# Optimization experiments

Hardware: AMD Instinct MI355X
Metric: run time of the kernel (lower is better)

The kernel has to match this reference:

```python
import jax, jax.numpy as jnp
import numpy as np

B, S, H, I, E = 4, 4096, 1024, 4096, 4
VOCAB = 32000


def setup_inputs() -> dict:
    key = jax.random.key(0)
    k1, k2, k3, k4, k5 = jax.random.split(key, 5)
    scale = 1.0 / np.sqrt(H)
    return {
        "hidden_states": jax.random.normal(k1, (B, S, H), dtype=jnp.float32),
        "gate_proj": jax.random.normal(k2, (E, H, I), dtype=jnp.float32) * scale,
        "up_proj": jax.random.normal(k3, (E, H, I), dtype=jnp.float32) * scale,
        "down_proj": jax.random.normal(k4, (E, I, H), dtype=jnp.float32) * (1.0 / np.sqrt(I)),
        "token_ids": jax.random.randint(k5, (B, S), 0, VOCAB, dtype=jnp.int64),
    }


def reference(hidden_states, gate_proj, up_proj, down_proj, token_ids):
    # hidden_states: [B, S, H]; token_ids: [B, S]
    num_experts = gate_proj.shape[0]
    expert_ids = token_ids % num_experts  # [B, S]
    out = jnp.zeros_like(hidden_states)
    for e in range(num_experts):  # small fixed expert loop
        gate = jax.nn.silu(jnp.einsum("bsh,hi->bsi", hidden_states, gate_proj[e]))
        up = jnp.einsum("bsh,hi->bsi", hidden_states, up_proj[e])
        y = jnp.einsum("bsi,ih->bsh", gate * up, down_proj[e])
        out = jnp.where((expert_ids == e)[..., None], y, out)
    return out
```

## Files before the change

### kernel.cpp

```cpp
#include <hip/hip_runtime.h>

#define TOK    16384
#define HD     1024
#define ID     4096
#define NE     4
#define MAXMT  131
#define MAXMT2 67

typedef __attribute__((ext_vector_type(4))) float f32x4;
typedef __attribute__((ext_vector_type(8))) short bf16x8;
typedef unsigned int u32;

static __device__ __forceinline__ unsigned short f2bf(float f) {
  unsigned u = __float_as_uint(f);
  u += 0x7FFFu + ((u >> 16) & 1u);
  return (unsigned short)(u >> 16);
}

static __device__ __forceinline__ void gl16(const void* g, void* l) {
  __builtin_amdgcn_global_load_lds((const __attribute__((address_space(1))) u32*)g,
                                   (__attribute__((address_space(3))) u32*)l, 16, 0, 0);
}

static __device__ __forceinline__ void barx() {
  asm volatile("" ::: "memory");
  __builtin_amdgcn_s_barrier();
  asm volatile("" ::: "memory");
}

__global__ void k_route0(const int* __restrict__ ids, int* __restrict__ meta) {
  __shared__ int cnt[4];
  int t = threadIdx.x;
  if (t < 4) cnt[t] = 0;
  __syncthreads();
  int l0 = 0, l1 = 0, l2 = 0, l3 = 0;
  for (int i = t; i < TOK; i += 256) {
    int e = ids[i] & 3;
    l0 += (e == 0); l1 += (e == 1); l2 += (e == 2); l3 += (e == 3);
  }
  atomicAdd(&cnt[0], l0); atomicAdd(&cnt[1], l1);
  atomicAdd(&cnt[2], l2); atomicAdd(&cnt[3], l3);
  __syncthreads();
  if (t == 0) {
    int o = 0;
    for (int e = 0; e < 4; ++e) { meta[e] = o; meta[8 + e] = o; o += cnt[e]; }
    meta[4] = o;
  }
}

__global__ void k_route1(const int* __restrict__ ids, int* __restrict__ meta,
                         int* __restrict__ perm) {
  int i = blockIdx.x * 256 + threadIdx.x;
  if (i < TOK) {
    int e = ids[i] & 3;
    int s = atomicAdd(&meta[8 + e], 1);
    perm[s] = i;
  }
}

__global__ void k_conv(const float* __restrict__ s, unsigned short* __restrict__ d, int n8) {
  int i = blockIdx.x * blockDim.x + threadIdx.x;
  int st = gridDim.x * blockDim.x;
  for (; i < n8; i += st) {
    const f32x4* p = (const f32x4*)(s + ((size_t)i << 3));
    f32x4 a = p[0], b = p[1];
    union { unsigned short u[8]; uint4 q; } o;
    o.u[0] = f2bf(a.x); o.u[1] = f2bf(a.y); o.u[2] = f2bf(a.z); o.u[3] = f2bf(a.w);
    o.u[4] = f2bf(b.x); o.u[5] = f2bf(b.y); o.u[6] = f2bf(b.z); o.u[7] = f2bf(b.w);
    *(uint4*)(d + ((size_t)i << 3)) = o.q;
  }
}

__global__ void k_tr(const float* __restrict__ src, unsigned short* __restrict__ dst,
                     int R, int C) {
  __shared__ float tile[64][65];
  size_t mo = (size_t)blockIdx.z * R * C;
  const float* s = src + mo;
  unsigned short* d = dst + mo;
  int r0 = blockIdx.y << 6, c0 = blockIdx.x << 6;
  int t = threadIdx.x;
  int lr = t >> 4, lc = (t & 15) << 2;
  #pragma unroll
  for (int it = 0; it < 4; ++it) {
    int r = lr + (it << 4);
    f32x4 v = *(const f32x4*)(s + (size_t)(r0 + r) * C + c0 + lc);
    tile[r][lc] = v.x; tile[r][lc + 1] = v.y; tile[r][lc + 2] = v.z; tile[r][lc + 3] = v.w;
  }
  __syncthreads();
  int c = t >> 2, rb = (t & 3) << 4;
  union { unsigned short u[16]; uint4 q[2]; } o;
  #pragma unroll
  for (int j = 0; j < 16; ++j) o.u[j] = f2bf(tile[rb + j][c]);
  uint4* dp = (uint4*)(d + (size_t)(c0 + c) * R + r0 + rb);
  dp[0] = o.q[0]; dp[1] = o.q[1];
}

#define MFMA16 __builtin_amdgcn_mfma_f32_16x16x32_bf16

__global__ __launch_bounds__(512, 2) void k_gemm1(
    const unsigned short* __restrict__ hid,
    const unsigned short* __restrict__ gT,
    const unsigned short* __restrict__ uT,
    const int* __restrict__ meta,
    const int* __restrict__ perm,
    unsigned short* __restrict__ act) {
  extern __shared__ __align__(16) char smem[];
  int offs[5];
  #pragma unroll
  for (int i = 0; i < 5; ++i) offs[i] = meta[i];
  int mt = blockIdx.x;
  int e = -1, mloc = 0, base = 0;
  #pragma unroll
  for (int ee = 0; ee < 4; ++ee) {
    int tiles = (offs[ee + 1] - offs[ee] + 255) >> 8;
    if (e < 0 && mt < base + tiles) { e = ee; mloc = mt - base; }
    base += tiles;
  }
  if (e < 0) return;
  int slot0 = offs[e] + (mloc << 8);
  int send = offs[e + 1];
  int tid = threadIdx.x, lane = tid & 63, wid = tid >> 6;
  int n0 = blockIdx.y << 7;

  int ke = (((tid & 7) ^ ((tid >> 3) & 7)) << 3);
  int rloc = tid >> 3;
  const unsigned short* srcA[4];
  #pragma unroll
  for (int i = 0; i < 4; ++i) {
    int slot = slot0 + i * 64 + rloc;
    int pr = perm[slot < send ? slot : slot0];
    srcA[i] = hid + (size_t)pr * HD + ke;
  }
  const unsigned short* gb = gT + (size_t)e * ID * HD;
  const unsigned short* ub = uT + (size_t)e * ID * HD;
  const unsigned short* srcG[2];
  const unsigned short* srcU[2];
  #pragma unroll
  for (int i = 0; i < 2; ++i) {
    int row = n0 + i * 64 + rloc;
    srcG[i] = gb + (size_t)row * HD + ke;
    srcU[i] = ub + (size_t)row * HD + ke;
  }
  int dstA[4], dstG[2], dstU[2];
  #pragma unroll
  for (int i = 0; i < 4; ++i) dstA[i] = i * 8192 + wid * 1024;
  #pragma unroll
  for (int i = 0; i < 2; ++i) { dstG[i] = 32768 + i * 8192 + wid * 1024;
                                dstU[i] = 49152 + i * 8192 + wid * 1024; }

  int wm = wid >> 1, wn = wid & 1;
  int r16 = lane & 15, kg = lane >> 4;
  int offA[4], offG[4], offU[4];
  #pragma unroll
  for (int m = 0; m < 4; ++m) {
    int row = wm * 64 + m * 16 + r16;
    offA[m] = row * 128 + ((kg << 4) ^ ((row & 7) << 4));
  }
  #pragma unroll
  for (int n = 0; n < 4; ++n) {
    int row = wn * 64 + n * 16 + r16;
    int o = row * 128 + ((kg << 4) ^ ((row & 7) << 4));
    offG[n] = 32768 + o;
    offU[n] = 49152 + o;
  }

  f32x4 zero = {0.f, 0.f, 0.f, 0.f};
  f32x4 ag[4][4], au[4][4];
  #pragma unroll
  for (int m = 0; m < 4; ++m)
    #pragma unroll
    for (int n = 0; n < 4; ++n) { ag[m][n] = zero; au[m][n] = zero; }

  {
    char* b = smem;
    #pragma unroll
    for (int i = 0; i < 4; ++i) gl16(srcA[i], b + dstA[i]);
    #pragma unroll
    for (int i = 0; i < 2; ++i) gl16(srcG[i], b + dstG[i]);
    #pragma unroll
    for (int i = 0; i < 2; ++i) gl16(srcU[i], b + dstU[i]);
  }

  #pragma unroll 2
  for (int t = 0; t < HD / 64; ++t) {
    const char* bc = smem + (t & 1) * 65536;
    if (t < HD / 64 - 1) {
      char* bn = smem + ((t + 1) & 1) * 65536;
      int ko = (t + 1) * 64;
      #pragma unroll
      for (int i = 0; i < 4; ++i) gl16(srcA[i] + ko, bn + dstA[i]);
      #pragma unroll
      for (int i = 0; i < 2; ++i) gl16(srcG[i] + ko, bn + dstG[i]);
      #pragma unroll
      for (int i = 0; i < 2; ++i) gl16(srcU[i] + ko, bn + dstU[i]);
      asm volatile("s_waitcnt vmcnt(8)" ::: "memory");
    } else {
      asm volatile("s_waitcnt vmcnt(0)" ::: "memory");
    }
    barx();

    bf16x8 fa[4], fg[4], fu[4];
    #pragma unroll
    for (int m = 0; m < 4; ++m) fa[m] = *(const bf16x8*)(bc + offA[m]);
    #pragma unroll
    for (int n = 0; n < 4; ++n) fg[n] = *(const bf16x8*)(bc + offG[n]);
    barx();
    asm volatile("s_waitcnt lgkmcnt(0)" ::: "memory");
    __builtin_amdgcn_sched_barrier(0);
    __builtin_amdgcn_s_setprio(1);
    #pragma unroll
    for (int m = 0; m < 4; ++m)
      #pragma unroll
      for (int n = 0; n < 4; ++n)
        ag[m][n] = MFMA16(fa[m], fg[n], ag[m][n], 0, 0, 0);
    __builtin_amdgcn_s_setprio(0);
    barx();
    #pragma unroll
    for (int n = 0; n < 4; ++n) fu[n] = *(const bf16x8*)(bc + offU[n]);
    barx();
    asm volatile("s_waitcnt lgkmcnt(0)" ::: "memory");
    __builtin_amdgcn_sched_barrier(0);
    __builtin_amdgcn_s_setprio(1);
    #pragma unroll
    for (int m = 0; m < 4; ++m)
      #pragma unroll
      for (int n = 0; n < 4; ++n)
        au[m][n] = MFMA16(fa[m], fu[n], au[m][n], 0, 0, 0);
    __builtin_amdgcn_s_setprio(0);
    barx();
    #pragma unroll
    for (int m = 0; m < 4; ++m) fa[m] = *(const bf16x8*)(bc + (offA[m] ^ 64));
    #pragma unroll
    for (int n = 0; n < 4; ++n) fg[n] = *(const bf16x8*)(bc + (offG[n] ^ 64));
    barx();
    asm volatile("s_waitcnt lgkmcnt(0)" ::: "memory");
    __builtin_amdgcn_sched_barrier(0);
    __builtin_amdgcn_s_setprio(1);
    #pragma unroll
    for (int m = 0; m < 4; ++m)
      #pragma unroll
      for (int n = 0; n < 4; ++n)
        ag[m][n] = MFMA16(fa[m], fg[n], ag[m][n], 0, 0, 0);
    __builtin_amdgcn_s_setprio(0);
    barx();
    #pragma unroll
    for (int n = 0; n < 4; ++n) fu[n] = *(const bf16x8*)(bc + (offU[n] ^ 64));
    barx();
    asm volatile("s_waitcnt lgkmcnt(0)" ::: "memory");
    __builtin_amdgcn_sched_barrier(0);
    __builtin_amdgcn_s_setprio(1);
    #pragma unroll
    for (int m = 0; m < 4; ++m)
      #pragma unroll
      for (int n = 0; n < 4; ++n)
        au[m][n] = MFMA16(fa[m], fu[n], au[m][n], 0, 0, 0);
    __builtin_amdgcn_s_setprio(0);
    barx();
  }

  #pragma unroll
  for (int m = 0; m < 4; ++m) {
    int lr = wm * 64 + m * 16 + kg * 4;
    #pragma unroll
    for (int n = 0; n < 4; ++n) {
      int col = n0 + wn * 64 + n * 16 + r16;
      #pragma unroll
      for (int r = 0; r < 4; ++r) {
        int slot = slot0 + lr + r;
        if (slot < send) {
          float g = ag[m][n][r];
          float u = au[m][n][r];
          float y = (g / (1.f + __expf(-g))) * u;
          act[(size_t)slot * ID + col] = f2bf(y);
        }
      }
    }
  }
}

__global__ __launch_bounds__(256, 2) void k_gemm2(
    const unsigned short* __restrict__ act,
    const unsigned short* __restrict__ dT,
    const int* __restrict__ meta,
    const int* __restrict__ perm,
    float* __restrict__ out) {
  __shared__ unsigned short As[128 * 64];
  __shared__ unsigned short Bs[128 * 64];
  int offs[5];
  #pragma unroll
  for (int i = 0; i < 5; ++i) offs[i] = meta[i];
  int mt = blockIdx.x;
  int e = -1, mloc = 0, base = 0;
  #pragma unroll
  for (int ee = 0; ee < 4; ++ee) {
    int tiles = (offs[ee + 1] - offs[ee] + 127) >> 7;
    if (e < 0 && mt < base + tiles) { e = ee; mloc = mt - base; }
    base += tiles;
  }
  if (e < 0) return;
  int slot0 = offs[e] + (mloc << 7);
  int send = offs[e + 1];
  int tid = threadIdx.x;
  int n0 = blockIdx.y << 7;
  const unsigned short* dbase = dT + (size_t)e * HD * ID;
  const unsigned short* ap[4];
  const unsigned short* bp[4];
  int wofs[4];
  #pragma unroll
  for (int it = 0; it < 4; ++it) {
    int b = (tid << 4) + (it << 12);
    int row = b >> 7;
    int kob = b & 127;
    int slot = slot0 + row;
    int s2 = slot < send ? slot : slot0;
    ap[it] = act + (size_t)s2 * ID + (kob >> 1);
    bp[it] = dbase + (size_t)(n0 + row) * ID + (kob >> 1);
    wofs[it] = row * 64 + ((kob ^ ((row & 7) << 4)) >> 1);
  }
  int lane = tid & 63, wid = tid >> 6;
  int wm = wid >> 1, wn = wid & 1;
  int r16 = lane & 15, kg = lane >> 4;
  f32x4 zero = {0.f, 0.f, 0.f, 0.f};
  f32x4 acc[4][4];
  #pragma unroll
  for (int m = 0; m < 4; ++m)
    #pragma unroll
    for (int n = 0; n < 4; ++n) acc[m][n] = zero;

  bf16x8 sa[4], sb[4];
  #pragma unroll
  for (int it = 0; it < 4; ++it) {
    sa[it] = *(const bf16x8*)(ap[it]);
    sb[it] = *(const bf16x8*)(bp[it]);
  }
  for (int kt = 0; kt < ID / 64; ++kt) {
    __syncthreads();
    #pragma unroll
    for (int it = 0; it < 4; ++it) {
      *(bf16x8*)(As + wofs[it]) = sa[it];
      *(bf16x8*)(Bs + wofs[it]) = sb[it];
    }
    __syncthreads();
    if (kt < ID / 64 - 1) {
      int ko = (kt + 1) << 6;
      #pragma unroll
      for (int it = 0; it < 4; ++it) {
        sa[it] = *(const bf16x8*)(ap[it] + ko);
        sb[it] = *(const bf16x8*)(bp[it] + ko);
      }
    }
    #pragma unroll
    for (int kk = 0; kk < 2; ++kk) {
      bf16x8 fa[4], fb[4];
      #pragma unroll
      for (int m = 0; m < 4; ++m) {
        int row = (wm << 6) + (m << 4) + r16;
        int kob = (kk << 6) + (kg << 4);
        fa[m] = *(const bf16x8*)(As + row * 64 + ((kob ^ ((row & 7) << 4)) >> 1));
      }
      #pragma unroll
      for (int n = 0; n < 4; ++n) {
        int row = (wn << 6) + (n << 4) + r16;
        int kob = (kk << 6) + (kg << 4);
        fb[n] = *(const bf16x8*)(Bs + row * 64 + ((kob ^ ((row & 7) << 4)) >> 1));
      }
      #pragma unroll
      for (int m = 0; m < 4; ++m)
        #pragma unroll
        for (int n = 0; n < 4; ++n)
          acc[m][n] = __builtin_amdgcn_mfma_f32_16x16x32_bf16(fa[m], fb[n], acc[m][n], 0, 0, 0);
    }
  }
  #pragma unroll
  for (int m = 0; m < 4; ++m) {
    int lr = (wm << 6) + (m << 4) + (kg << 2);
    int pr4[4];
    #pragma unroll
    for (int r = 0; r < 4; ++r) {
      int slot = slot0 + lr + r;
      pr4[r] = slot < send ? perm[slot] : -1;
    }
    #pragma unroll
    for (int n = 0; n < 4; ++n) {
      int col = n0 + (wn << 6) + (n << 4) + r16;
      #pragma unroll
      for (int r = 0; r < 4; ++r) {
        if (pr4[r] >= 0) out[(size_t)pr4[r] * HD + col] = acc[m][n][r];
      }
    }
  }
}

extern "C" void kernel_launch(void* const* d_in, const int* in_sizes, int n_in,
                              void* d_out, int out_size, void* d_ws, size_t ws_size,
                              hipStream_t stream) {
  const float* hs = (const float*)d_in[0];
  const float* gw = (const float*)d_in[1];
  const float* uw = (const float*)d_in[2];
  const float* dw = (const float*)d_in[3];
  const int* ids = (const int*)d_in[4];
  float* out = (float*)d_out;

  char* w = (char*)d_ws;
  size_t o = 0;
  int* meta = (int*)(w + o); o += 64;
  int* perm = (int*)(w + o); o += (size_t)TOK * 4;
  o = (o + 255) & ~(size_t)255;
  unsigned short* hid = (unsigned short*)(w + o); o += (size_t)TOK * HD * 2;
  unsigned short* gT  = (unsigned short*)(w + o); o += (size_t)NE * ID * HD * 2;
  unsigned short* uT  = (unsigned short*)(w + o); o += (size_t)NE * ID * HD * 2;
  unsigned short* dT  = (unsigned short*)(w + o); o += (size_t)NE * ID * HD * 2;
  unsigned short* actb = (unsigned short*)(w + o); o += (size_t)TOK * ID * 2;

  hipFuncSetAttribute((const void*)k_gemm1,
                      hipFuncAttributeMaxDynamicSharedMemorySize, 131072);

  hipLaunchKernelGGL(k_route0, dim3(1), dim3(256), 0, stream, ids, meta);
  hipLaunchKernelGGL(k_route1, dim3(TOK / 256), dim3(256), 0, stream, ids, meta, perm);
  hipLaunchKernelGGL(k_conv, dim3(2048), dim3(256), 0, stream, hs, hid, TOK * HD / 8);
  hipLaunchKernelGGL(k_tr, dim3(ID / 64, HD / 64, NE), dim3(256), 0, stream, gw, gT, HD, ID);
  hipLaunchKernelGGL(k_tr, dim3(ID / 64, HD / 64, NE), dim3(256), 0, stream, uw, uT, HD, ID);
  hipLaunchKernelGGL(k_tr, dim3(HD / 64, ID / 64, NE), dim3(256), 0, stream, dw, dT, ID, HD);
  hipLaunchKernelGGL(k_gemm1, dim3(MAXMT2, ID / 128), dim3(512), 131072, stream,
                     hid, gT, uT, meta, perm, actb);
  hipLaunchKernelGGL(k_gemm2, dim3(MAXMT, HD / 128), dim3(256), 0, stream,
                     actb, dT, meta, perm, out);
}
```

Before: 767.7 us.

## Restructure gate/up GEMM into unified 256x256 tile with interleaved staging

The gate and up weight tiles are interleaved into one B operand, so each wave computes a 128x64 output block with 8x4 accumulators. Global-to-LDS staging is split into half-tile pieces and interleaved between MFMA phases within a manually unrolled double-buffered loop. Both GEMMs now use a 1-D grid remapped so that consecutive blocks are spread across 8 groups (XCD-aware swizzle) for better L2 reuse. The three transpose launches are merged into a single kernel. Register pressure and tricky waitcnt accounting are the main risks.

```diff
diff --git a/kernel.cpp b/kernel.cpp
--- a/kernel.cpp
+++ b/kernel.cpp
@@ -6,6 +6,7 @@
 #define NE     4
 #define MAXMT  131
 #define MAXMT2 67
+#define NKT    (HD / 64)
 
 typedef __attribute__((ext_vector_type(4))) float f32x4;
 typedef __attribute__((ext_vector_type(8))) short bf16x8;
@@ -71,13 +72,25 @@
   }
 }
 
-__global__ void k_tr(const float* __restrict__ src, unsigned short* __restrict__ dst,
-                     int R, int C) {
+__global__ void k_tr12(const float* __restrict__ gw, const float* __restrict__ uw,
+                       const float* __restrict__ dw, unsigned short* __restrict__ gT,
+                       unsigned short* __restrict__ uT, unsigned short* __restrict__ dT) {
   __shared__ float tile[64][65];
-  size_t mo = (size_t)blockIdx.z * R * C;
-  const float* s = src + mo;
-  unsigned short* d = dst + mo;
-  int r0 = blockIdx.y << 6, c0 = blockIdx.x << 6;
+  int z = blockIdx.y;
+  const float* s; unsigned short* d; int R, C, lg;
+  if (z < 8) {
+    R = HD; C = ID; lg = 6;
+    int m = z & 3;
+    if (z < 4) { s = gw + (size_t)m * R * C; d = gT + (size_t)m * R * C; }
+    else       { s = uw + (size_t)m * R * C; d = uT + (size_t)m * R * C; }
+  } else {
+    R = ID; C = HD; lg = 4;
+    int m = z - 8;
+    s = dw + (size_t)m * R * C; d = dT + (size_t)m * R * C;
+  }
+  int bx = blockIdx.x;
+  int tx = bx & ((1 << lg) - 1), ty = bx >> lg;
+  int r0 = ty << 6, c0 = tx << 6;
   int t = threadIdx.x;
   int lr = t >> 4, lc = (t & 15) << 2;
   #pragma unroll
@@ -96,6 +109,23 @@
 }
 
 #define MFMA16 __builtin_amdgcn_mfma_f32_16x16x32_bf16
+
+#define RD_A(MH, KX, D) { _Pragma("unroll") for (int m = 0; m < 4; ++m) \
+  fa[m] = *(const bf16x8*)(smem + (D) + ((offA[m] + (MH) * 8192) ^ ((KX) << 6))); }
+#define RD_B(KX, D) { _Pragma("unroll") for (int n = 0; n < 4; ++n) \
+  fb[n] = *(const bf16x8*)(smem + (D) + (offB[n] ^ ((KX) << 6))); }
+#define STG_A(HH, TILE, D) { _Pragma("unroll") for (int j = (HH) * 2; j < (HH) * 2 + 2; ++j) \
+  gl16(srcA[j] + (TILE) * 64, smem + (D) + dstA[j]); }
+#define STG_B(HH, TILE, D) { _Pragma("unroll") for (int j = (HH) * 2; j < (HH) * 2 + 2; ++j) \
+  gl16(srcB[j] + (TILE) * 64, smem + (D) + dstB[j]); }
+#define PH_TAIL(MH) barx(); \
+  asm volatile("s_waitcnt lgkmcnt(0)" ::: "memory"); \
+  __builtin_amdgcn_sched_barrier(0); \
+  __builtin_amdgcn_s_setprio(1); \
+  { _Pragma("unroll") for (int m = 0; m < 4; ++m) \
+    _Pragma("unroll") for (int n = 0; n < 4; ++n) \
+      acc[(MH) * 4 + m][n] = MFMA16(fa[m], fb[n], acc[(MH) * 4 + m][n], 0, 0, 0); } \
+  __builtin_amdgcn_s_setprio(0)
 
 __global__ __launch_bounds__(512, 2) void k_gemm1(
     const unsigned short* __restrict__ hid,
@@ -108,7 +138,10 @@
   int offs[5];
   #pragma unroll
   for (int i = 0; i < 5; ++i) offs[i] = meta[i];
-  int mt = blockIdx.x;
+  int bid = blockIdx.x;
+  int logical = (bid & 7) * (MAXMT2 * 32 / 8) + (bid >> 3);
+  int mt = logical >> 5;
+  int ny = logical & 31;
   int e = -1, mloc = 0, base = 0;
   #pragma unroll
   for (int ee = 0; ee < 4; ++ee) {
@@ -120,156 +153,122 @@
   int slot0 = offs[e] + (mloc << 8);
   int send = offs[e + 1];
   int tid = threadIdx.x, lane = tid & 63, wid = tid >> 6;
-  int n0 = blockIdx.y << 7;
-
-  int ke = (((tid & 7) ^ ((tid >> 3) & 7)) << 3);
-  int rloc = tid >> 3;
+  int n0 = ny << 7;
+
+  int rsub = lane >> 3;
+  int ke = ((lane & 7) ^ rsub) << 3;
   const unsigned short* srcA[4];
-  #pragma unroll
-  for (int i = 0; i < 4; ++i) {
-    int slot = slot0 + i * 64 + rloc;
-    int pr = perm[slot < send ? slot : slot0];
-    srcA[i] = hid + (size_t)pr * HD + ke;
-  }
+  const unsigned short* srcB[4];
+  int dstA[4], dstB[4];
   const unsigned short* gb = gT + (size_t)e * ID * HD;
   const unsigned short* ub = uT + (size_t)e * ID * HD;
-  const unsigned short* srcG[2];
-  const unsigned short* srcU[2];
-  #pragma unroll
-  for (int i = 0; i < 2; ++i) {
-    int row = n0 + i * 64 + rloc;
-    srcG[i] = gb + (size_t)row * HD + ke;
-    srcU[i] = ub + (size_t)row * HD + ke;
-  }
-  int dstA[4], dstG[2], dstU[2];
-  #pragma unroll
-  for (int i = 0; i < 4; ++i) dstA[i] = i * 8192 + wid * 1024;
-  #pragma unroll
-  for (int i = 0; i < 2; ++i) { dstG[i] = 32768 + i * 8192 + wid * 1024;
-                                dstU[i] = 49152 + i * 8192 + wid * 1024; }
-
-  int wm = wid >> 1, wn = wid & 1;
+  #pragma unroll
+  for (int j = 0; j < 4; ++j) {
+    int r = j * 64 + wid * 8 + rsub;
+    int slot = slot0 + r;
+    int pr = perm[slot < send ? slot : slot0];
+    srcA[j] = hid + (size_t)pr * HD + ke;
+    dstA[j] = j * 8192 + wid * 1024;
+    int rb = r;
+    int s = rb >> 4;
+    int grow = n0 + ((s >> 1) << 4) + (rb & 15);
+    srcB[j] = ((s & 1) ? ub : gb) + (size_t)grow * HD + ke;
+    dstB[j] = 32768 + j * 8192 + wid * 1024;
+  }
+
+  int wm = wid >> 2, wn = wid & 3;
   int r16 = lane & 15, kg = lane >> 4;
-  int offA[4], offG[4], offU[4];
+  int offA[4], offB[4];
   #pragma unroll
   for (int m = 0; m < 4; ++m) {
-    int row = wm * 64 + m * 16 + r16;
+    int row = wm * 128 + m * 16 + r16;
     offA[m] = row * 128 + ((kg << 4) ^ ((row & 7) << 4));
   }
   #pragma unroll
   for (int n = 0; n < 4; ++n) {
     int row = wn * 64 + n * 16 + r16;
-    int o = row * 128 + ((kg << 4) ^ ((row & 7) << 4));
-    offG[n] = 32768 + o;
-    offU[n] = 49152 + o;
-  }
-
-  f32x4 zero = {0.f, 0.f, 0.f, 0.f};
-  f32x4 ag[4][4], au[4][4];
-  #pragma unroll
-  for (int m = 0; m < 4; ++m)
-    #pragma unroll
-    for (int n = 0; n < 4; ++n) { ag[m][n] = zero; au[m][n] = zero; }
-
+    offB[n] = 32768 + row * 128 + ((kg << 4) ^ ((row & 7) << 4));
+  }
+
+  f32x4 acc[8][4];
+  #pragma unroll
+  for (int m = 0; m < 8; ++m)
+    #pragma unroll
+    for (int n = 0; n < 4; ++n) acc[m][n] = (f32x4){0.f, 0.f, 0.f, 0.f};
+  bf16x8 fa[4], fb[4];
+
+  STG_B(0, 0, 0);
+  STG_A(0, 0, 0); STG_A(1, 0, 0);
+  STG_B(1, 0, 0);
+  STG_B(0, 1, 65536);
+  asm volatile("s_waitcnt vmcnt(2)" ::: "memory");
+  barx();
+
+  #pragma unroll 1
+  for (int i = 0; i < NKT / 2 - 1; ++i) {
+    int t1 = 2 * i + 1, t2 = 2 * i + 2, t3 = 2 * i + 3;
+    RD_A(0, 0, 0); RD_B(0, 0);
+    STG_B(1, t1, 65536);
+    PH_TAIL(0); barx();
+    RD_A(1, 0, 0);
+    STG_A(0, t1, 65536); STG_A(1, t1, 65536);
+    PH_TAIL(1); barx();
+    RD_A(0, 1, 0); RD_B(1, 0);
+    PH_TAIL(0); barx();
+    RD_A(1, 1, 0);
+    STG_B(0, t2, 0);
+    PH_TAIL(1);
+    asm volatile("s_waitcnt vmcnt(2)" ::: "memory");
+    barx();
+    RD_A(0, 0, 65536); RD_B(0, 65536);
+    STG_A(0, t2, 0); STG_A(1, t2, 0);
+    PH_TAIL(0); barx();
+    RD_A(1, 0, 65536);
+    STG_B(1, t2, 0);
+    PH_TAIL(1); barx();
+    RD_A(0, 1, 65536); RD_B(1, 65536);
+    PH_TAIL(0); barx();
+    RD_A(1, 1, 65536);
+    STG_B(0, t3, 65536);
+    PH_TAIL(1);
+    asm volatile("s_waitcnt vmcnt(2)" ::: "memory");
+    barx();
+  }
   {
-    char* b = smem;
-    #pragma unroll
-    for (int i = 0; i < 4; ++i) gl16(srcA[i], b + dstA[i]);
-    #pragma unroll
-    for (int i = 0; i < 2; ++i) gl16(srcG[i], b + dstG[i]);
-    #pragma unroll
-    for (int i = 0; i < 2; ++i) gl16(srcU[i], b + dstU[i]);
-  }
-
-  #pragma unroll 2
-  for (int t = 0; t < HD / 64; ++t) {
-    const char* bc = smem + (t & 1) * 65536;
-    if (t < HD / 64 - 1) {
-      char* bn = smem + ((t + 1) & 1) * 65536;
-      int ko = (t + 1) * 64;
-      #pragma unroll
-      for (int i = 0; i < 4; ++i) gl16(srcA[i] + ko, bn + dstA[i]);
-      #pragma unroll
-      for (int i = 0; i < 2; ++i) gl16(srcG[i] + ko, bn + dstG[i]);
-      #pragma unroll
-      for (int i = 0; i < 2; ++i) gl16(srcU[i] + ko, bn + dstU[i]);
-      asm volatile("s_waitcnt vmcnt(8)" ::: "memory");
-    } else {
-      asm volatile("s_waitcnt vmcnt(0)" ::: "memory");
-    }
+    RD_A(0, 0, 0); RD_B(0, 0);
+    STG_B(1, 15, 65536);
+    PH_TAIL(0); barx();
+    RD_A(1, 0, 0);
+    STG_A(0, 15, 65536); STG_A(1, 15, 65536);
+    PH_TAIL(1); barx();
+    RD_A(0, 1, 0); RD_B(1, 0);
+    PH_TAIL(0); barx();
+    RD_A(1, 1, 0);
+    PH_TAIL(1);
+    asm volatile("s_waitcnt vmcnt(0)" ::: "memory");
     barx();
-
-    bf16x8 fa[4], fg[4], fu[4];
-    #pragma unroll
-    for (int m = 0; m < 4; ++m) fa[m] = *(const bf16x8*)(bc + offA[m]);
-    #pragma unroll
-    for (int n = 0; n < 4; ++n) fg[n] = *(const bf16x8*)(bc + offG[n]);
-    barx();
-    asm volatile("s_waitcnt lgkmcnt(0)" ::: "memory");
-    __builtin_amdgcn_sched_barrier(0);
-    __builtin_amdgcn_s_setprio(1);
-    #pragma unroll
-    for (int m = 0; m < 4; ++m)
-      #pragma unroll
-      for (int n = 0; n < 4; ++n)
-        ag[m][n] = MFMA16(fa[m], fg[n], ag[m][n], 0, 0, 0);
-    __builtin_amdgcn_s_setprio(0);
-    barx();
-    #pragma unroll
-    for (int n = 0; n < 4; ++n) fu[n] = *(const bf16x8*)(bc + offU[n]);
-    barx();
-    asm volatile("s_waitcnt lgkmcnt(0)" ::: "memory");
-    __builtin_amdgcn_sched_barrier(0);
-    __builtin_amdgcn_s_setprio(1);
-    #pragma unroll
-    for (int m = 0; m < 4; ++m)
-      #pragma unroll
-      for (int n = 0; n < 4; ++n)
-        au[m][n] = MFMA16(fa[m], fu[n], au[m][n], 0, 0, 0);
-    __builtin_amdgcn_s_setprio(0);
-    barx();
-    #pragma unroll
-    for (int m = 0; m < 4; ++m) fa[m] = *(const bf16x8*)(bc + (offA[m] ^ 64));
-    #pragma unroll
-    for (int n = 0; n < 4; ++n) fg[n] = *(const bf16x8*)(bc + (offG[n] ^ 64));
-    barx();
-    asm volatile("s_waitcnt lgkmcnt(0)" ::: "memory");
-    __builtin_amdgcn_sched_barrier(0);
-    __builtin_amdgcn_s_setprio(1);
-    #pragma unroll
-    for (int m = 0; m < 4; ++m)
-      #pragma unroll
-      for (int n = 0; n < 4; ++n)
-        ag[m][n] = MFMA16(fa[m], fg[n], ag[m][n], 0, 0, 0);
-    __builtin_amdgcn_s_setprio(0);
-    barx();
-    #pragma unroll
-    for (int n = 0; n < 4; ++n) fu[n] = *(const bf16x8*)(bc + (offU[n] ^ 64));
-    barx();
-    asm volatile("s_waitcnt lgkmcnt(0)" ::: "memory");
-    __builtin_amdgcn_sched_barrier(0);
-    __builtin_amdgcn_s_setprio(1);
-    #pragma unroll
-    for (int m = 0; m < 4; ++m)
-      #pragma unroll
-      for (int n = 0; n < 4; ++n)
-        au[m][n] = MFMA16(fa[m], fu[n], au[m][n], 0, 0, 0);
-    __builtin_amdgcn_s_setprio(0);
-    barx();
-  }
-
-  #pragma unroll
-  for (int m = 0; m < 4; ++m) {
-    int lr = wm * 64 + m * 16 + kg * 4;
-    #pragma unroll
-    for (int n = 0; n < 4; ++n) {
-      int col = n0 + wn * 64 + n * 16 + r16;
+    RD_A(0, 0, 65536); RD_B(0, 65536);
+    PH_TAIL(0); barx();
+    RD_A(1, 0, 65536);
+    PH_TAIL(1); barx();
+    RD_A(0, 1, 65536); RD_B(1, 65536);
+    PH_TAIL(0); barx();
+    RD_A(1, 1, 65536);
+    PH_TAIL(1);
+  }
+
+  #pragma unroll
+  for (int mf = 0; mf < 8; ++mf) {
+    int lr = wm * 128 + mf * 16 + kg * 4;
+    #pragma unroll
+    for (int np = 0; np < 2; ++np) {
+      int col = n0 + (2 * wn + np) * 16 + r16;
       #pragma unroll
       for (int r = 0; r < 4; ++r) {
         int slot = slot0 + lr + r;
         if (slot < send) {
-          float g = ag[m][n][r];
-          float u = au[m][n][r];
+          float g = acc[mf][2 * np][r];
+          float u = acc[mf][2 * np + 1][r];
           float y = (g / (1.f + __expf(-g))) * u;
           act[(size_t)slot * ID + col] = f2bf(y);
         }
@@ -289,7 +288,10 @@
   int offs[5];
   #pragma unroll
   for (int i = 0; i < 5; ++i) offs[i] = meta[i];
-  int mt = blockIdx.x;
+  int bid = blockIdx.x;
+  int logical = (bid & 7) * (MAXMT * 8 / 8) + (bid >> 3);
+  int mt = logical >> 3;
+  int nyy = logical & 7;
   int e = -1, mloc = 0, base = 0;
   #pragma unroll
   for (int ee = 0; ee < 4; ++ee) {
@@ -301,7 +303,7 @@
   int slot0 = offs[e] + (mloc << 7);
   int send = offs[e + 1];
   int tid = threadIdx.x;
-  int n0 = blockIdx.y << 7;
+  int n0 = nyy << 7;
   const unsigned short* dbase = dT + (size_t)e * HD * ID;
   const unsigned short* ap[4];
   const unsigned short* bp[4];
@@ -418,11 +420,9 @@
   hipLaunchKernelGGL(k_route0, dim3(1), dim3(256), 0, stream, ids, meta);
   hipLaunchKernelGGL(k_route1, dim3(TOK / 256), dim3(256), 0, stream, ids, meta, perm);
   hipLaunchKernelGGL(k_conv, dim3(2048), dim3(256), 0, stream, hs, hid, TOK * HD / 8);
-  hipLaunchKernelGGL(k_tr, dim3(ID / 64, HD / 64, NE), dim3(256), 0, stream, gw, gT, HD, ID);
-  hipLaunchKernelGGL(k_tr, dim3(ID / 64, HD / 64, NE), dim3(256), 0, stream, uw, uT, HD, ID);
-  hipLaunchKernelGGL(k_tr, dim3(HD / 64, ID / 64, NE), dim3(256), 0, stream, dw, dT, ID, HD);
-  hipLaunchKernelGGL(k_gemm1, dim3(MAXMT2, ID / 128), dim3(512), 131072, stream,
+  hipLaunchKernelGGL(k_tr12, dim3(1024, 12), dim3(256), 0, stream, gw, uw, dw, gT, uT, dT);
+  hipLaunchKernelGGL(k_gemm1, dim3(MAXMT2 * 32), dim3(512), 131072, stream,
                      hid, gT, uT, meta, perm, actb);
-  hipLaunchKernelGGL(k_gemm2, dim3(MAXMT, HD / 128), dim3(256), 0, stream,
+  hipLaunchKernelGGL(k_gemm2, dim3(MAXMT * 8), dim3(256), 0, stream,
                      actb, dT, meta, perm, out);
 }
```

After: 666.9 us. 1.15x faster.
